# Performance work log

Hardware: AMD Instinct MI355X
Metric: run time of the kernel (lower is better)

The kernel has to match this reference:

```python
import jax, jax.numpy as jnp
import numpy as np

HIDDEN = 4096
NUM_EXPERTS = 64
TOPK = 2
N_TOKENS = 16384


def setup_inputs() -> dict:
    key = jax.random.key(0)
    k_x, k_w, k_b = jax.random.split(key, 3)
    x = jax.random.normal(k_x, (N_TOKENS, HIDDEN), dtype=jnp.float32)
    # torch.nn.Linear: weight [out, in], bias [out], uniform(-1/sqrt(in), 1/sqrt(in))
    bound = 1.0 / np.sqrt(HIDDEN)
    W = jax.random.uniform(k_w, (NUM_EXPERTS, HIDDEN), dtype=jnp.float32, minval=-bound, maxval=bound)
    b = jax.random.uniform(k_b, (NUM_EXPERTS,), dtype=jnp.float32, minval=-bound, maxval=bound)
    return {"x": x, "W": W, "b": b}


def reference(x, W, b):
    # logits: [N, E] = x @ W.T + b
    logits = jnp.einsum("nh,eh->ne", x, W) + b
    probs = jax.nn.softmax(logits, axis=1)
    # torch.topk along dim=1 returns (values, indices), sorted descending
    values, indices = jax.lax.top_k(probs, TOPK)
    return values, indices
```

## Files before the change

### kernel.cpp

```cpp
#include <hip/hip_runtime.h>
#include <math.h>

#define HIDDEN   4096
#define NEXP     64
#define NTOK     16384
#define KCHUNKS  8
#define KC       (HIDDEN / KCHUNKS)
#define BK       16
#define ITERS    (KC / BK)
#define BT       64

__global__ __launch_bounds__(128, 4)
void gemm_partial(const float* __restrict__ x, const float* __restrict__ W,
                  float* __restrict__ part) {
    __shared__ float lds[2][2][64 * BK];

    const int tid  = threadIdx.x;
    const int lane = tid & 63;
    const int eh   = tid >> 6;
    const int t0   = blockIdx.x * BT;
    const int kbase = blockIdx.y * KC;
    const int i = lane >> 3;
    const int j = lane & 7;

    const int srow = lane >> 2;
    const int sevn = 4 * ((lane & 3) ^ ((lane >> 5) & 3));
    const int sodd = 4 * ((lane & 3) ^ ((2 + (lane >> 5)) & 3));
    const float* sbase = (eh == 0) ? (x + (size_t)t0 * HIDDEN) : W;

#define STAGE(buf, itn) do {                                                          \
    _Pragma("unroll")                                                                 \
    for (int p = 0; p < 4; ++p) {                                                     \
        const int ko = kbase + (itn) * BK + ((p & 1) ? sodd : sevn);                  \
        __builtin_amdgcn_global_load_lds(                                             \
            (const __attribute__((address_space(1))) uint32_t*)                       \
                (sbase + (size_t)(p * 16 + srow) * HIDDEN + ko),                      \
            (__attribute__((address_space(3))) uint32_t*)&lds[buf][eh][p * 256],      \
            16, 0, 0);                                                                \
    }                                                                                 \
} while (0)

    float acc[8][4];
#pragma unroll
    for (int m = 0; m < 8; ++m)
#pragma unroll
        for (int e = 0; e < 4; ++e) acc[m][e] = 0.f;

    STAGE(0, 0);
    __syncthreads();

    for (int it = 0; it < ITERS; ++it) {
        const int cb = it & 1;
        if (it + 1 < ITERS) STAGE(cb ^ 1, it + 1);

#pragma unroll
        for (int g = 0; g < 4; ++g) {
            float4 WV[4];
#pragma unroll
            for (int e = 0; e < 4; ++e) {
                const int rw = eh * 32 + j * 4 + e;
                WV[e] = *(const float4*)&lds[cb][1][rw * BK + 4 * (g ^ ((rw >> 3) & 3))];
            }
#pragma unroll
            for (int m = 0; m < 8; ++m) {
                const int rx = i * 8 + m;
                const float4 xq = *(const float4*)&lds[cb][0][rx * BK + 4 * (g ^ ((rx >> 3) & 3))];
#pragma unroll
                for (int e = 0; e < 4; ++e) {
                    float a = fmaf(xq.x, WV[e].x, acc[m][e]);
                    a       = fmaf(xq.y, WV[e].y, a);
                    a       = fmaf(xq.z, WV[e].z, a);
                    acc[m][e] = fmaf(xq.w, WV[e].w, a);
                }
            }
        }
        __syncthreads();
    }
#undef STAGE

    float* dst = part + ((size_t)blockIdx.y * NTOK + t0) * NEXP + eh * 32;
#pragma unroll
    for (int m = 0; m < 8; ++m) {
        const int tok = i * 8 + m;
        *(float4*)&dst[(size_t)tok * NEXP + j * 4] =
            make_float4(acc[m][0], acc[m][1], acc[m][2], acc[m][3]);
    }
}

__global__ __launch_bounds__(256)
void softmax_top2(const float* __restrict__ part, const float* __restrict__ bias,
                  float* __restrict__ out) {
    const int lane = threadIdx.x & 63;
    const int wid  = threadIdx.x >> 6;
    const int t    = blockIdx.x * 4 + wid;

    float l = bias[lane];
#pragma unroll
    for (int c = 0; c < KCHUNKS; ++c)
        l += part[((size_t)c * NTOK + t) * NEXP + lane];

    float m = l;
#pragma unroll
    for (int s = 32; s > 0; s >>= 1)
        m = fmaxf(m, __shfl_xor(m, s, 64));

    float ssum = expf(l - m);
#pragma unroll
    for (int s = 32; s > 0; s >>= 1)
        ssum += __shfl_xor(ssum, s, 64);

    float v1 = l; int i1 = lane;
#pragma unroll
    for (int s = 32; s > 0; s >>= 1) {
        float ov = __shfl_xor(v1, s, 64);
        int   oi = __shfl_xor(i1, s, 64);
        if (ov > v1 || (ov == v1 && oi < i1)) { v1 = ov; i1 = oi; }
    }
    float v2 = (lane == i1) ? -INFINITY : l;
    int   i2 = lane;
#pragma unroll
    for (int s = 32; s > 0; s >>= 1) {
        float ov = __shfl_xor(v2, s, 64);
        int   oi = __shfl_xor(i2, s, 64);
        if (ov > v2 || (ov == v2 && oi < i2)) { v2 = ov; i2 = oi; }
    }

    if (lane == 0) {
        const float inv = 1.0f / ssum;
        out[(size_t)t * 2 + 0] = inv;
        out[(size_t)t * 2 + 1] = expf(v2 - m) * inv;
        out[(size_t)2 * NTOK + t * 2 + 0] = (float)i1;
        out[(size_t)2 * NTOK + t * 2 + 1] = (float)i2;
    }
}

extern "C" void kernel_launch(void* const* d_in, const int* in_sizes, int n_in,
                              void* d_out, int out_size, void* d_ws, size_t ws_size,
                              hipStream_t stream) {
    const float* x  = (const float*)d_in[0];
    const float* W  = (const float*)d_in[1];
    const float* b  = (const float*)d_in[2];
    float* out  = (float*)d_out;
    float* part = (float*)d_ws;

    dim3 g1(NTOK / BT, KCHUNKS);
    gemm_partial<<<g1, 128, 0, stream>>>(x, W, part);
    softmax_top2<<<NTOK / 4, 256, 0, stream>>>(part, b, out);
}
```

Before: 457.8 us.

## Transpose W once and read it via scalar loads, one token per lane

A small kernel now writes W transposed to [K, E] in the workspace. The GEMM maps one token to each lane and 16 experts to each wave. Only x is staged in LDS, and the W rows are wave-uniform, so they can come through scalar or broadcast loads instead of LDS. This cuts LDS traffic and rebalances the register tile, at the cost of an extra transpose launch and more dependence on the scalar cache.

```diff
diff --git a/kernel.cpp b/kernel.cpp
--- a/kernel.cpp
+++ b/kernel.cpp
@@ -6,45 +6,49 @@
 #define NTOK     16384
 #define KCHUNKS  8
 #define KC       (HIDDEN / KCHUNKS)
-#define BK       16
+#define BK       32
 #define ITERS    (KC / BK)
 #define BT       64
 
-__global__ __launch_bounds__(128, 4)
-void gemm_partial(const float* __restrict__ x, const float* __restrict__ W,
+__global__ void wtrans(const float* __restrict__ W, float* __restrict__ Wt) {
+    const int k  = blockIdx.x * 64 + (threadIdx.x & 63);
+    const int e0 = threadIdx.x >> 6;
+#pragma unroll
+    for (int ee = 0; ee < 64; ee += 4)
+        Wt[(size_t)k * NEXP + (ee + e0)] = W[(size_t)(ee + e0) * HIDDEN + k];
+}
+
+__global__ __launch_bounds__(256, 8)
+void gemm_partial(const float* __restrict__ x, const float* __restrict__ Wt,
                   float* __restrict__ part) {
-    __shared__ float lds[2][2][64 * BK];
+    __shared__ float lds[2][64 * BK];
 
-    const int tid  = threadIdx.x;
-    const int lane = tid & 63;
-    const int eh   = tid >> 6;
-    const int t0   = blockIdx.x * BT;
+    const int tid   = threadIdx.x;
+    const int lane  = tid & 63;
+    const int wid   = __builtin_amdgcn_readfirstlane(tid >> 6);
+    const int ebase = wid * 16;
+    const int t0    = blockIdx.x * BT;
     const int kbase = blockIdx.y * KC;
-    const int i = lane >> 3;
-    const int j = lane & 7;
 
-    const int srow = lane >> 2;
-    const int sevn = 4 * ((lane & 3) ^ ((lane >> 5) & 3));
-    const int sodd = 4 * ((lane & 3) ^ ((2 + (lane >> 5)) & 3));
-    const float* sbase = (eh == 0) ? (x + (size_t)t0 * HIDDEN) : W;
+    const int srow = lane >> 3;
+    const int sko  = 4 * ((lane & 7) ^ ((lane >> 3) & 7));
 
 #define STAGE(buf, itn) do {                                                          \
     _Pragma("unroll")                                                                 \
-    for (int p = 0; p < 4; ++p) {                                                     \
-        const int ko = kbase + (itn) * BK + ((p & 1) ? sodd : sevn);                  \
+    for (int p = 0; p < 2; ++p) {                                                     \
         __builtin_amdgcn_global_load_lds(                                             \
             (const __attribute__((address_space(1))) uint32_t*)                       \
-                (sbase + (size_t)(p * 16 + srow) * HIDDEN + ko),                      \
-            (__attribute__((address_space(3))) uint32_t*)&lds[buf][eh][p * 256],      \
+                (x + (size_t)(t0 + wid * 16 + p * 8 + srow) * HIDDEN                  \
+                   + kbase + (itn) * BK + sko),                                       \
+            (__attribute__((address_space(3))) uint32_t*)                             \
+                &lds[buf][wid * 512 + p * 256],                                       \
             16, 0, 0);                                                                \
     }                                                                                 \
 } while (0)
 
-    float acc[8][4];
+    float acc[16];
 #pragma unroll
-    for (int m = 0; m < 8; ++m)
-#pragma unroll
-        for (int e = 0; e < 4; ++e) acc[m][e] = 0.f;
+    for (int e = 0; e < 16; ++e) acc[e] = 0.f;
 
     STAGE(0, 0);
     __syncthreads();
@@ -52,39 +56,31 @@
     for (int it = 0; it < ITERS; ++it) {
         const int cb = it & 1;
         if (it + 1 < ITERS) STAGE(cb ^ 1, it + 1);
+        const int k0 = kbase + it * BK;
 
 #pragma unroll
-        for (int g = 0; g < 4; ++g) {
-            float4 WV[4];
+        for (int g = 0; g < 8; ++g) {
+            const float4 xq = *(const float4*)&lds[cb][lane * 32 + 4 * (g ^ (lane & 7))];
 #pragma unroll
-            for (int e = 0; e < 4; ++e) {
-                const int rw = eh * 32 + j * 4 + e;
-                WV[e] = *(const float4*)&lds[cb][1][rw * BK + 4 * (g ^ ((rw >> 3) & 3))];
-            }
+            for (int dk = 0; dk < 4; ++dk) {
+                const float xs = (dk == 0) ? xq.x : (dk == 1) ? xq.y
+                               : (dk == 2) ? xq.z : xq.w;
+                const float* __restrict__ wrow =
+                    Wt + (size_t)(k0 + g * 4 + dk) * NEXP + ebase;
 #pragma unroll
-            for (int m = 0; m < 8; ++m) {
-                const int rx = i * 8 + m;
-                const float4 xq = *(const float4*)&lds[cb][0][rx * BK + 4 * (g ^ ((rx >> 3) & 3))];
-#pragma unroll
-                for (int e = 0; e < 4; ++e) {
-                    float a = fmaf(xq.x, WV[e].x, acc[m][e]);
-                    a       = fmaf(xq.y, WV[e].y, a);
-                    a       = fmaf(xq.z, WV[e].z, a);
-                    acc[m][e] = fmaf(xq.w, WV[e].w, a);
-                }
+                for (int e = 0; e < 16; ++e)
+                    acc[e] = fmaf(xs, wrow[e], acc[e]);
             }
         }
         __syncthreads();
     }
 #undef STAGE
 
-    float* dst = part + ((size_t)blockIdx.y * NTOK + t0) * NEXP + eh * 32;
+    float* dst = part + ((size_t)blockIdx.y * NTOK + t0 + lane) * NEXP + ebase;
 #pragma unroll
-    for (int m = 0; m < 8; ++m) {
-        const int tok = i * 8 + m;
-        *(float4*)&dst[(size_t)tok * NEXP + j * 4] =
-            make_float4(acc[m][0], acc[m][1], acc[m][2], acc[m][3]);
-    }
+    for (int h = 0; h < 4; ++h)
+        *(float4*)&dst[h * 4] =
+            make_float4(acc[h * 4 + 0], acc[h * 4 + 1], acc[h * 4 + 2], acc[h * 4 + 3]);
 }
 
 __global__ __launch_bounds__(256)
@@ -142,8 +138,10 @@
     const float* b  = (const float*)d_in[2];
     float* out  = (float*)d_out;
     float* part = (float*)d_ws;
+    float* Wt   = part + (size_t)KCHUNKS * NTOK * NEXP;
 
+    wtrans<<<dim3(HIDDEN / 64), 256, 0, stream>>>(W, Wt);
     dim3 g1(NTOK / BT, KCHUNKS);
-    gemm_partial<<<g1, 128, 0, stream>>>(x, W, part);
+    gemm_partial<<<g1, 256, 0, stream>>>(x, Wt, part);
     softmax_top2<<<NTOK / 4, 256, 0, stream>>>(part, b, out);
 }
```

Result: faster. 428.1 us (-6.5%).
